# Kernel tuning notes

Hardware: AMD Instinct MI355X
Metric: run time of the kernel (lower is better)

The kernel has to match this reference:

```python
import jax, jax.numpy as jnp
import numpy as np

A, B, D, L = 256, 64, 768, 2  # annotators, batch, hidden, num_labels
G1, G2 = 4, 8                 # groups per attribute


def setup_inputs() -> dict:
    key = jax.random.key(0)
    ks = jax.random.split(key, 9)
    s = 1.0 / np.sqrt(D)
    return {
        "pooled": jax.random.normal(ks[0], (B, D), jnp.float32),
        "W1": jax.random.normal(ks[1], (G1, D, D), jnp.float32) * s,
        "b1": jax.random.normal(ks[2], (G1, D), jnp.float32) * s,
        "W2": jax.random.normal(ks[3], (G2, D, D), jnp.float32) * s,
        "b2": jax.random.normal(ks[4], (G2, D), jnp.float32) * s,
        "Wh": jax.random.normal(ks[5], (A, D, L), jnp.float32) * s,
        "bh": jax.random.normal(ks[6], (A, L), jnp.float32) * s,
        "g1_idx": jax.random.randint(ks[7], (A,), 0, G1),
        "g2_idx": jax.random.randint(ks[8], (A,), 0, G2),
    }


def reference(pooled, W1, b1, W2, b2, Wh, bh, g1_idx, g2_idx):
    # Attribute 1: every annotator with the same group shares the transform,
    # so compute once per group then gather (avoids A redundant GEMMs).
    h_g = jnp.einsum('bd,gde->gbe', pooled, W1) + b1[:, None, :]   # [G1, B, D]
    h = h_g[g1_idx]                                                # [A, B, D]
    # Attribute 2: input now differs per annotator -> grouped GEMM via gathered weights.
    h = jnp.einsum('abd,ade->abe', h, W2[g2_idx]) + b2[g2_idx][:, None, :]  # [A, B, D]
    # Per-annotator classification heads.
    logits = jnp.einsum('abd,adl->abl', h, Wh) + bh[:, None, :]    # [A, B, L]
    # Match torch layout: logits[batch, annotator, label]
    return jnp.transpose(logits, (1, 0, 2))                        # [B, A, L]
```

## Files before the change

kernel.cpp:

```cpp
#include <hip/hip_runtime.h>
#include <hip/hip_bf16.h>

#define AN 256
#define BN 64
#define DN 768
#define LN 2
#define G1N 4
#define G2N 8
#define KI (DN / 32)

typedef __attribute__((ext_vector_type(8))) short short8;
typedef __attribute__((ext_vector_type(4))) short bf16x4;
typedef __attribute__((ext_vector_type(4))) float floatx4;

static __device__ __forceinline__ unsigned short f2bf(float f) {
    union { float f; unsigned int u; } v; v.f = f;
    unsigned int r = v.u + 0x7FFF + ((v.u >> 16) & 1);
    return (unsigned short)(r >> 16);
}

__global__ __launch_bounds__(256) void k_prep(
    const float* __restrict__ pooled,
    const float* __restrict__ b2, const float* __restrict__ Wh,
    const float* __restrict__ bh,
    const int* __restrict__ g1i, const int* __restrict__ g2i,
    unsigned short* __restrict__ Whp,
    unsigned short* __restrict__ pooled_bf, float* __restrict__ bc,
    int* __restrict__ n1, int* __restrict__ n2,
    int* __restrict__ lst1, int* __restrict__ sidx2)
{
    const int tid = threadIdx.x, bx = blockIdx.x;

    if (bx < 8) {
        const int i0 = bx * 6144;
        for (int i = i0 + tid; i < i0 + 6144; i += 256)
            pooled_bf[i] = f2bf(pooled[i]);

        const int aa = tid >> 3, j = tid & 7;
        const int a = bx * 32 + aa;
        const int gv2 = g2i[a];
        const float* whp = Wh + (size_t)a * (DN * LN);
        const float* b2p = b2 + gv2 * DN;
        float acc0 = 0.f, acc1 = 0.f;
        #pragma unroll 4
        for (int i = 0; i < 48; ++i) {
            int e = j * 96 + i * 2;
            float4 w4 = *(const float4*)(whp + e * 2);
            float2 bv = *(const float2*)(b2p + e);
            acc0 += bv.x * w4.x + bv.y * w4.z;
            acc1 += bv.x * w4.y + bv.y * w4.w;
        }
        #pragma unroll
        for (int off = 4; off; off >>= 1) {
            acc0 += __shfl_down(acc0, off, 64);
            acc1 += __shfl_down(acc1, off, 64);
        }
        if (j == 0) {
            bc[a * 2 + 0] = acc0 + bh[a * 2 + 0];
            bc[a * 2 + 1] = acc1 + bh[a * 2 + 1];
        }
        return;
    }

    if (bx == 8) {
        __shared__ int g1s[AN], g2s[AN];
        __shared__ int c1s[G1N], c2s[G2N];
        g1s[tid] = g1i[tid];
        g2s[tid] = g2i[tid];
        if (tid < G1N) c1s[tid] = 0;
        if (tid < G2N) c2s[tid] = 0;
        __syncthreads();
        int s = 0, my2 = g2s[tid];
        for (int a2 = 0; a2 < tid; ++a2) s += (g2s[a2] == my2);
        sidx2[tid] = s;
        atomicAdd(&c2s[my2], 1);
        int p1 = atomicAdd(&c1s[g1s[tid]], 1);
        lst1[g1s[tid] * 256 + p1] = tid;
        __syncthreads();
        if (tid < G1N) n1[tid] = c1s[tid];
        if (tid < G2N) n2[tid] = c2s[tid];
        return;
    }

    {
        const int a = bx - 9;
        __shared__ int g2s[AN];
        g2s[tid] = g2i[tid];
        __syncthreads();
        int s = 0, my2 = g2s[a];
        for (int a2 = 0; a2 < a; ++a2) s += (g2s[a2] == my2);
        const size_t rp = ((size_t)my2 * 128 + s) * 2;
        const float* wa = Wh + (size_t)a * (DN * LN);
        #pragma unroll
        for (int i = 0; i < 3; ++i) {
            int e = i * 256 + tid;
            float2 v = *(const float2*)(wa + e * 2);
            Whp[rp * DN + e]       = f2bf(v.x);
            Whp[(rp + 1) * DN + e] = f2bf(v.y);
        }
    }
}

__global__ __launch_bounds__(256) void k_mid(
    const float* __restrict__ W1, const float* __restrict__ W2,
    const float* __restrict__ b1,
    const unsigned short* __restrict__ Whp,
    const unsigned short* __restrict__ pooled_bf,
    const int* __restrict__ n2,
    unsigned short* __restrict__ h1, unsigned short* __restrict__ Wcs)
{
    const int tid  = threadIdx.x;
    const int lane = tid & 63, wave = tid >> 6;
    const int nn   = lane & 15, quad = lane >> 4;
    const int bx   = blockIdx.x;

    if (bx < 48) {
        const int g = bx / 12, e0 = (bx % 12) * 64;
        const int e = e0 + wave * 16 + nn;
        const float* Wcol = W1 + (size_t)g * DN * DN + e;
        const unsigned short* Ap = pooled_bf + (size_t)nn * DN + quad * 8;
        floatx4 acc[4] = {{0,0,0,0},{0,0,0,0},{0,0,0,0},{0,0,0,0}};
        #pragma unroll
        for (int kk = 0; kk < KI; ++kk) {
            const float* wk = Wcol + (size_t)(kk * 32 + quad * 8) * DN;
            short8 bf;
            #pragma unroll
            for (int j = 0; j < 8; ++j)
                bf[j] = (short)f2bf(wk[(size_t)j * DN]);
            #pragma unroll
            for (int mt = 0; mt < 4; ++mt) {
                short8 af = *(const short8*)(Ap + (size_t)(mt * 16) * DN + kk * 32);
                acc[mt] = __builtin_amdgcn_mfma_f32_16x16x32_bf16(af, bf, acc[mt], 0, 0, 0);
            }
        }
        const float bv = b1[g * DN + e];
        #pragma unroll
        for (int mt = 0; mt < 4; ++mt)
            #pragma unroll
            for (int r = 0; r < 4; ++r)
                h1[(size_t)g * BN * DN + (size_t)(mt * 16 + quad * 4 + r) * DN + e] =
                    f2bf(acc[mt][r] + bv);
    } else {
        const int j = bx - 48;
        const int g = j / 12;
        const int mbase = (j % 12) * 64;
        const int cols = 2 * n2[g];
        const int m_row = mbase + wave * 16 + nn;

        const float* ap = W2 + ((size_t)g * DN + m_row) * DN + quad * 8;
        short8 Areg[KI];
        #pragma unroll
        for (int kk = 0; kk < KI; ++kk) {
            float4 a0 = *(const float4*)(ap + kk * 32);
            float4 a1 = *(const float4*)(ap + kk * 32 + 4);
            short8 af;
            af[0] = (short)f2bf(a0.x); af[1] = (short)f2bf(a0.y);
            af[2] = (short)f2bf(a0.z); af[3] = (short)f2bf(a0.w);
            af[4] = (short)f2bf(a1.x); af[5] = (short)f2bf(a1.y);
            af[6] = (short)f2bf(a1.z); af[7] = (short)f2bf(a1.w);
            Areg[kk] = af;
        }

        const unsigned short* Bbase = Whp + (size_t)(g * 256) * DN;
        for (int c0 = 0; c0 < cols; c0 += 16) {
            const unsigned short* Brow = Bbase + (size_t)(c0 + nn) * DN + quad * 8;
            floatx4 acc = {0, 0, 0, 0};
            #pragma unroll
            for (int kk = 0; kk < KI; ++kk) {
                short8 bf = *(const short8*)(Brow + kk * 32);
                acc = __builtin_amdgcn_mfma_f32_16x16x32_bf16(Areg[kk], bf, acc, 0, 0, 0);
            }
            const int c = c0 + nn;
            if (c < cols) {
                const int dbase = mbase + wave * 16 + quad * 4;
                bf16x4 v;
                #pragma unroll
                for (int r = 0; r < 4; ++r) v[r] = (short)f2bf(acc[r]);
                *(bf16x4*)(Wcs + (size_t)(g * 256 + c) * DN + dbase) = v;
            }
        }
    }
}

__global__ __launch_bounds__(256) void k_last(
    const unsigned short* __restrict__ h1, const unsigned short* __restrict__ Wcs,
    const float* __restrict__ bc, const int* __restrict__ n1,
    const int* __restrict__ lst1, const int* __restrict__ sidx2,
    const int* __restrict__ g2i, float* __restrict__ out)
{
    const int g = blockIdx.y;
    const int cols = 2 * n1[g];
    const int nt0 = blockIdx.x * 16;
    if (nt0 >= cols) return;

    const int tid = threadIdx.x;
    const int lane = tid & 63, wave = tid >> 6;
    const int nn = lane & 15, quad = lane >> 4;

    const int c = nt0 + nn;
    const bool valid = (c < cols);
    const int cl = valid ? c : (cols - 1);
    const int a = lst1[g * 256 + (cl >> 1)];
    const int l = cl & 1;
    const int rp = (g2i[a] * 128 + sidx2[a]) * 2 + l;

    const unsigned short* hg = h1 + (size_t)g * BN * DN + (size_t)(wave * 16 + nn) * DN + quad * 8;
    const unsigned short* wp = Wcs + (size_t)rp * DN + quad * 8;

    floatx4 acc = {0, 0, 0, 0};
    #pragma unroll
    for (int kk = 0; kk < KI; ++kk) {
        short8 af = *(const short8*)(hg + kk * 32);
        short8 bf = *(const short8*)(wp + kk * 32);
        acc = __builtin_amdgcn_mfma_f32_16x16x32_bf16(af, bf, acc, 0, 0, 0);
    }
    if (valid) {
        const float bv = bc[a * 2 + l];
        #pragma unroll
        for (int r = 0; r < 4; ++r)
            out[(size_t)(wave * 16 + quad * 4 + r) * (AN * LN) + a * 2 + l] = acc[r] + bv;
    }
}

extern "C" void kernel_launch(void* const* d_in, const int* in_sizes, int n_in,
                              void* d_out, int out_size, void* d_ws, size_t ws_size,
                              hipStream_t stream) {
    const float* pooled = (const float*)d_in[0];
    const float* W1     = (const float*)d_in[1];
    const float* b1     = (const float*)d_in[2];
    const float* W2     = (const float*)d_in[3];
    const float* b2     = (const float*)d_in[4];
    const float* Wh     = (const float*)d_in[5];
    const float* bh     = (const float*)d_in[6];
    const int*   g1i    = (const int*)d_in[7];
    const int*   g2i    = (const int*)d_in[8];
    float* out = (float*)d_out;

    char* ws = (char*)d_ws;
    float* bc   = (float*)ws;             ws += 512 * 4;
    int*   n1   = (int*)ws;               ws += 4 * 4;
    int*   n2   = (int*)ws;               ws += 8 * 4;
    int*   lst1 = (int*)ws;               ws += 4 * 256 * 4;
    int*   sidx2= (int*)ws;               ws += 256 * 4;
    unsigned short* pooled_bf = (unsigned short*)ws;  ws += (size_t)BN * DN * 2;
    unsigned short* h1        = (unsigned short*)ws;  ws += (size_t)G1N * BN * DN * 2;
    unsigned short* Whp       = (unsigned short*)ws;  ws += (size_t)G2N * 256 * DN * 2;
    unsigned short* Wcs       = (unsigned short*)ws;

    dim3 blk(256);
    k_prep<<<dim3(265),   blk, 0, stream>>>(pooled, b2, Wh, bh, g1i, g2i,
                                            Whp, pooled_bf, bc, n1, n2, lst1, sidx2);
    k_mid <<<dim3(144),   blk, 0, stream>>>(W1, W2, b1, Whp, pooled_bf, n2, h1, Wcs);
    k_last<<<dim3(32, 4), blk, 0, stream>>>(h1, Wcs, bc, n1, lst1, sidx2, g2i, out);
}
```

Before: 135.0 us.

## Fuse prep kernel into main GEMM kernel, staging inputs in LDS

Removes the separate prep launch. The W1 blocks now convert pooled to bf16 into padded shared memory. The W2 blocks build their per-group annotator list and convert Wh tiles to bf16 in LDS on the fly, and the head-bias computation moves into extra blocks of the same kernel. The last kernel recomputes group lists and ranks in shared memory instead of reading workspace index arrays. This cuts one launch and a global round trip, but each block repeats the pooled conversion and the O(A^2) rank scans, and adds syncthreads inside the column loop.

```diff
diff --git a/kernel.cpp b/kernel.cpp
--- a/kernel.cpp
+++ b/kernel.cpp
@@ -1,5 +1,4 @@
 #include <hip/hip_runtime.h>
-#include <hip/hip_bf16.h>
 
 #define AN 256
 #define BN 64
@@ -8,6 +7,7 @@
 #define G1N 4
 #define G2N 8
 #define KI (DN / 32)
+#define PAD 776
 
 typedef __attribute__((ext_vector_type(8))) short short8;
 typedef __attribute__((ext_vector_type(4))) short bf16x4;
@@ -18,107 +18,44 @@
     unsigned int r = v.u + 0x7FFF + ((v.u >> 16) & 1);
     return (unsigned short)(r >> 16);
 }
-
-__global__ __launch_bounds__(256) void k_prep(
-    const float* __restrict__ pooled,
+static __device__ __forceinline__ unsigned int pack2(float a, float b) {
+    return (unsigned int)f2bf(a) | ((unsigned int)f2bf(b) << 16);
+}
+
+__global__ __launch_bounds__(256) void k_main(
+    const float* __restrict__ pooled, const float* __restrict__ W1,
+    const float* __restrict__ b1, const float* __restrict__ W2,
     const float* __restrict__ b2, const float* __restrict__ Wh,
-    const float* __restrict__ bh,
-    const int* __restrict__ g1i, const int* __restrict__ g2i,
-    unsigned short* __restrict__ Whp,
-    unsigned short* __restrict__ pooled_bf, float* __restrict__ bc,
-    int* __restrict__ n1, int* __restrict__ n2,
-    int* __restrict__ lst1, int* __restrict__ sidx2)
+    const float* __restrict__ bh, const int* __restrict__ g2i,
+    unsigned short* __restrict__ h1, unsigned short* __restrict__ Wcs,
+    float* __restrict__ bc)
 {
+    __shared__ __align__(16) unsigned char smem[64 * PAD * 2];
     const int tid = threadIdx.x, bx = blockIdx.x;
-
-    if (bx < 8) {
-        const int i0 = bx * 6144;
-        for (int i = i0 + tid; i < i0 + 6144; i += 256)
-            pooled_bf[i] = f2bf(pooled[i]);
-
-        const int aa = tid >> 3, j = tid & 7;
-        const int a = bx * 32 + aa;
-        const int gv2 = g2i[a];
-        const float* whp = Wh + (size_t)a * (DN * LN);
-        const float* b2p = b2 + gv2 * DN;
-        float acc0 = 0.f, acc1 = 0.f;
-        #pragma unroll 4
-        for (int i = 0; i < 48; ++i) {
-            int e = j * 96 + i * 2;
-            float4 w4 = *(const float4*)(whp + e * 2);
-            float2 bv = *(const float2*)(b2p + e);
-            acc0 += bv.x * w4.x + bv.y * w4.z;
-            acc1 += bv.x * w4.y + bv.y * w4.w;
-        }
-        #pragma unroll
-        for (int off = 4; off; off >>= 1) {
-            acc0 += __shfl_down(acc0, off, 64);
-            acc1 += __shfl_down(acc1, off, 64);
-        }
-        if (j == 0) {
-            bc[a * 2 + 0] = acc0 + bh[a * 2 + 0];
-            bc[a * 2 + 1] = acc1 + bh[a * 2 + 1];
-        }
-        return;
-    }
-
-    if (bx == 8) {
-        __shared__ int g1s[AN], g2s[AN];
-        __shared__ int c1s[G1N], c2s[G2N];
-        g1s[tid] = g1i[tid];
-        g2s[tid] = g2i[tid];
-        if (tid < G1N) c1s[tid] = 0;
-        if (tid < G2N) c2s[tid] = 0;
+    const int lane = tid & 63, wave = tid >> 6;
+    const int nn = lane & 15, quad = lane >> 4;
+
+    if (bx < 48) {
+        unsigned short* ps = (unsigned short*)smem;
+        {
+            const float4* p4 = (const float4*)pooled;
+            #pragma unroll
+            for (int i = 0; i < 48; ++i) {
+                const int idx = i * 256 + tid;
+                float4 v = p4[idx];
+                const int row = idx / 192, c4 = idx % 192;
+                const unsigned long long w =
+                    (unsigned long long)pack2(v.x, v.y) |
+                    ((unsigned long long)pack2(v.z, v.w) << 32);
+                *(unsigned long long*)(ps + row * PAD + c4 * 4) = w;
+            }
+        }
         __syncthreads();
-        int s = 0, my2 = g2s[tid];
-        for (int a2 = 0; a2 < tid; ++a2) s += (g2s[a2] == my2);
-        sidx2[tid] = s;
-        atomicAdd(&c2s[my2], 1);
-        int p1 = atomicAdd(&c1s[g1s[tid]], 1);
-        lst1[g1s[tid] * 256 + p1] = tid;
-        __syncthreads();
-        if (tid < G1N) n1[tid] = c1s[tid];
-        if (tid < G2N) n2[tid] = c2s[tid];
-        return;
-    }
-
-    {
-        const int a = bx - 9;
-        __shared__ int g2s[AN];
-        g2s[tid] = g2i[tid];
-        __syncthreads();
-        int s = 0, my2 = g2s[a];
-        for (int a2 = 0; a2 < a; ++a2) s += (g2s[a2] == my2);
-        const size_t rp = ((size_t)my2 * 128 + s) * 2;
-        const float* wa = Wh + (size_t)a * (DN * LN);
-        #pragma unroll
-        for (int i = 0; i < 3; ++i) {
-            int e = i * 256 + tid;
-            float2 v = *(const float2*)(wa + e * 2);
-            Whp[rp * DN + e]       = f2bf(v.x);
-            Whp[(rp + 1) * DN + e] = f2bf(v.y);
-        }
-    }
-}
-
-__global__ __launch_bounds__(256) void k_mid(
-    const float* __restrict__ W1, const float* __restrict__ W2,
-    const float* __restrict__ b1,
-    const unsigned short* __restrict__ Whp,
-    const unsigned short* __restrict__ pooled_bf,
-    const int* __restrict__ n2,
-    unsigned short* __restrict__ h1, unsigned short* __restrict__ Wcs)
-{
-    const int tid  = threadIdx.x;
-    const int lane = tid & 63, wave = tid >> 6;
-    const int nn   = lane & 15, quad = lane >> 4;
-    const int bx   = blockIdx.x;
-
-    if (bx < 48) {
+
         const int g = bx / 12, e0 = (bx % 12) * 64;
         const int e = e0 + wave * 16 + nn;
         const float* Wcol = W1 + (size_t)g * DN * DN + e;
-        const unsigned short* Ap = pooled_bf + (size_t)nn * DN + quad * 8;
+        const unsigned short* Ap = ps + nn * PAD + quad * 8;
         floatx4 acc[4] = {{0,0,0,0},{0,0,0,0},{0,0,0,0},{0,0,0,0}};
         #pragma unroll
         for (int kk = 0; kk < KI; ++kk) {
@@ -129,7 +66,7 @@
                 bf[j] = (short)f2bf(wk[(size_t)j * DN]);
             #pragma unroll
             for (int mt = 0; mt < 4; ++mt) {
-                short8 af = *(const short8*)(Ap + (size_t)(mt * 16) * DN + kk * 32);
+                short8 af = *(const short8*)(Ap + (mt * 16) * PAD + kk * 32);
                 acc[mt] = __builtin_amdgcn_mfma_f32_16x16x32_bf16(af, bf, acc[mt], 0, 0, 0);
             }
         }
@@ -140,13 +77,14 @@
             for (int r = 0; r < 4; ++r)
                 h1[(size_t)g * BN * DN + (size_t)(mt * 16 + quad * 4 + r) * DN + e] =
                     f2bf(acc[mt][r] + bv);
-    } else {
-        const int j = bx - 48;
-        const int g = j / 12;
-        const int mbase = (j % 12) * 64;
-        const int cols = 2 * n2[g];
+    } else if (bx < 144) {
+        int* g2s  = (int*)smem;
+        int* lst2 = (int*)(smem + 1024);
+        unsigned short* Whs = (unsigned short*)(smem + 2048);
+
+        const int j = bx - 48, g = j / 12, mbase = (j % 12) * 64;
+
         const int m_row = mbase + wave * 16 + nn;
-
         const float* ap = W2 + ((size_t)g * DN + m_row) * DN + quad * 8;
         short8 Areg[KI];
         #pragma unroll
@@ -161,9 +99,34 @@
             Areg[kk] = af;
         }
 
-        const unsigned short* Bbase = Whp + (size_t)(g * 256) * DN;
+        g2s[tid] = g2i[tid];
+        __syncthreads();
+        const int my = g2s[tid];
+        int rk = 0;
+        for (int a2 = 0; a2 < tid; ++a2) rk += (g2s[a2] == my);
+        if (my == g) lst2[rk] = tid;
+        int n2g = 0;
+        for (int a2 = 0; a2 < AN; ++a2) n2g += (g2s[a2] == g);
+        __syncthreads();
+        const int cols = 2 * n2g;
+
+        const int al = tid >> 5, t32 = tid & 31;
         for (int c0 = 0; c0 < cols; c0 += 16) {
-            const unsigned short* Brow = Bbase + (size_t)(c0 + nn) * DN + quad * 8;
+            const int sidx = (c0 >> 1) + al;
+            if (sidx < n2g) {
+                const int a = lst2[sidx];
+                const float4* wa4 = (const float4*)(Wh + (size_t)a * (DN * LN));
+                #pragma unroll
+                for (int i = 0; i < 12; ++i) {
+                    const int f4 = i * 32 + t32;
+                    float4 v = wa4[f4];
+                    const int e2 = f4 * 2;
+                    *(unsigned int*)(Whs + (2 * al)     * PAD + e2) = pack2(v.x, v.z);
+                    *(unsigned int*)(Whs + (2 * al + 1) * PAD + e2) = pack2(v.y, v.w);
+                }
+            }
+            __syncthreads();
+            const unsigned short* Brow = Whs + nn * PAD + quad * 8;
             floatx4 acc = {0, 0, 0, 0};
             #pragma unroll
             for (int kk = 0; kk < KI; ++kk) {
@@ -178,31 +141,72 @@
                 for (int r = 0; r < 4; ++r) v[r] = (short)f2bf(acc[r]);
                 *(bf16x4*)(Wcs + (size_t)(g * 256 + c) * DN + dbase) = v;
             }
-        }
-    }
-}
-
-__global__ __launch_bounds__(256) void k_last(
+            __syncthreads();
+        }
+    } else {
+        const int jb = bx - 144;
+        const int aa = tid >> 3, jj = tid & 7;
+        const int a = jb * 32 + aa;
+        const int gv2 = g2i[a];
+        const float* whp = Wh + (size_t)a * (DN * LN);
+        const float* b2p = b2 + gv2 * DN;
+        float acc0 = 0.f, acc1 = 0.f;
+        #pragma unroll 4
+        for (int i = 0; i < 48; ++i) {
+            int e = jj * 96 + i * 2;
+            float4 w4 = *(const float4*)(whp + e * 2);
+            float2 bv = *(const float2*)(b2p + e);
+            acc0 += bv.x * w4.x + bv.y * w4.z;
+            acc1 += bv.x * w4.y + bv.y * w4.w;
+        }
+        #pragma unroll
+        for (int off = 4; off; off >>= 1) {
+            acc0 += __shfl_down(acc0, off, 64);
+            acc1 += __shfl_down(acc1, off, 64);
+        }
+        if (jj == 0) {
+            bc[a * 2 + 0] = acc0 + bh[a * 2 + 0];
+            bc[a * 2 + 1] = acc1 + bh[a * 2 + 1];
+        }
+    }
+}
+
+__global__ __launch_bounds__(256) void k_out(
     const unsigned short* __restrict__ h1, const unsigned short* __restrict__ Wcs,
-    const float* __restrict__ bc, const int* __restrict__ n1,
-    const int* __restrict__ lst1, const int* __restrict__ sidx2,
+    const float* __restrict__ bc, const int* __restrict__ g1i,
     const int* __restrict__ g2i, float* __restrict__ out)
 {
+    __shared__ int g1s[AN], g2s[AN], lst1[AN], sx2[AN];
     const int g = blockIdx.y;
-    const int cols = 2 * n1[g];
+    const int tid = threadIdx.x;
+    g1s[tid] = g1i[tid];
+    g2s[tid] = g2i[tid];
+    __syncthreads();
+    const int m1 = g1s[tid], m2 = g2s[tid];
+    int r1 = 0, r2 = 0;
+    for (int a2 = 0; a2 < tid; ++a2) {
+        r1 += (g1s[a2] == m1);
+        r2 += (g2s[a2] == m2);
+    }
+    sx2[tid] = r2;
+    if (m1 == g) lst1[r1] = tid;
+    int n1g = 0;
+    for (int a2 = 0; a2 < AN; ++a2) n1g += (g1s[a2] == g);
+    __syncthreads();
+
+    const int cols = 2 * n1g;
     const int nt0 = blockIdx.x * 16;
     if (nt0 >= cols) return;
 
-    const int tid = threadIdx.x;
     const int lane = tid & 63, wave = tid >> 6;
     const int nn = lane & 15, quad = lane >> 4;
 
     const int c = nt0 + nn;
     const bool valid = (c < cols);
     const int cl = valid ? c : (cols - 1);
-    const int a = lst1[g * 256 + (cl >> 1)];
+    const int a = lst1[cl >> 1];
     const int l = cl & 1;
-    const int rp = (g2i[a] * 128 + sidx2[a]) * 2 + l;
+    const int rp = (g2s[a] * 128 + sx2[a]) * 2 + l;
 
     const unsigned short* hg = h1 + (size_t)g * BN * DN + (size_t)(wave * 16 + nn) * DN + quad * 8;
     const unsigned short* wp = Wcs + (size_t)rp * DN + quad * 8;
@@ -237,19 +241,12 @@
     float* out = (float*)d_out;
 
     char* ws = (char*)d_ws;
-    float* bc   = (float*)ws;             ws += 512 * 4;
-    int*   n1   = (int*)ws;               ws += 4 * 4;
-    int*   n2   = (int*)ws;               ws += 8 * 4;
-    int*   lst1 = (int*)ws;               ws += 4 * 256 * 4;
-    int*   sidx2= (int*)ws;               ws += 256 * 4;
-    unsigned short* pooled_bf = (unsigned short*)ws;  ws += (size_t)BN * DN * 2;
-    unsigned short* h1        = (unsigned short*)ws;  ws += (size_t)G1N * BN * DN * 2;
-    unsigned short* Whp       = (unsigned short*)ws;  ws += (size_t)G2N * 256 * DN * 2;
-    unsigned short* Wcs       = (unsigned short*)ws;
+    float* bc = (float*)ws;                           ws += 512 * 4;
+    unsigned short* h1  = (unsigned short*)ws;        ws += (size_t)G1N * BN * DN * 2;
+    unsigned short* Wcs = (unsigned short*)ws;
 
     dim3 blk(256);
-    k_prep<<<dim3(265),   blk, 0, stream>>>(pooled, b2, Wh, bh, g1i, g2i,
-                                            Whp, pooled_bf, bc, n1, n2, lst1, sidx2);
-    k_mid <<<dim3(144),   blk, 0, stream>>>(W1, W2, b1, Whp, pooled_bf, n2, h1, Wcs);
-    k_last<<<dim3(32, 4), blk, 0, stream>>>(h1, Wcs, bc, n1, lst1, sidx2, g2i, out);
-}
+    k_main<<<dim3(152),   blk, 0, stream>>>(pooled, W1, b1, W2, b2, Wh, bh, g2i,
+                                            h1, Wcs, bc);
+    k_out <<<dim3(32, 4), blk, 0, stream>>>(h1, Wcs, bc, g1i, g2i, out);
+}
```

New measurement: 116.4 us. 1.16x faster.
